# Kernel optimization log

Hardware: AMD Instinct MI355X
Metric: run time of the kernel (lower is better)

Reference implementation:

```python
import jax, jax.numpy as jnp
import numpy as np

T, IN, H, OUT = 4096, 1024, 2048, 1024


def setup_inputs() -> dict:
    key = jax.random.key(0)
    ks = jax.random.split(key, 7)
    s_x = np.float32(np.sqrt(2.0 / (IN + H)))   # Wx init scale
    s_h = np.float32(np.sqrt(1.0 / H))          # Wh init scale
    s_y = np.float32(np.sqrt(2.0 / (H + OUT)))  # Wy init scale
    return {
        "x": jax.random.normal(ks[0], (T, IN), jnp.float32),
        "Wx_f": jax.random.normal(ks[1], (H, IN), jnp.float32) * s_x,
        "Wh_f": jax.random.normal(ks[2], (H, H), jnp.float32) * s_h,
        "bh_f": jnp.zeros((H,), jnp.float32),
        "Wx_b": jax.random.normal(ks[3], (H, IN), jnp.float32) * s_x,
        "Wh_b": jax.random.normal(ks[4], (H, H), jnp.float32) * s_h,
        "bh_b": jnp.zeros((H,), jnp.float32),
        "Wy_f": jax.random.normal(ks[5], (OUT, H), jnp.float32) * s_y,
        "Wy_b": jax.random.normal(ks[6], (OUT, H), jnp.float32) * s_y,
        "by": jnp.zeros((OUT,), jnp.float32),
    }


def reference(x, Wx_f, Wh_f, bh_f, Wx_b, Wh_b, bh_b, Wy_f, Wy_b, by):
    # Precompute input projections for all timesteps (batched GEMM): [T, H]
    xWf = x @ Wx_f.T + bh_f
    xWb = x @ Wx_b.T + bh_b
    h0 = jnp.zeros((Wh_f.shape[0],), x.dtype)

    def make_step(Wh):
        def step(h, xw):
            h = jnp.tanh(xw + h @ Wh.T)
            return h, h
        return step

    # Forward direction: h_t = tanh(Wx x_t + Wh h_{t-1} + bh)
    _, hf = jax.lax.scan(make_step(Wh_f), h0, xWf)
    # Backward direction: same recurrence scanned from t=T-1 down to 0;
    # reverse=True yields outputs stacked in original time order,
    # matching h_backward_hist[::-1] in the torch code.
    _, hb = jax.lax.scan(make_step(Wh_b), h0, xWb, reverse=True)

    # Output per timestep: Wy_f h_f + Wy_b h_b + by -> [T, OUT], flattened
    y = hf @ Wy_f.T + hb @ Wy_b.T + by
    return y.reshape(-1)
```

## Files before the change

kernel.cpp:

```cpp
#include <hip/hip_runtime.h>
#include <hip/hip_bf16.h>
#include <math.h>

#define T_N   4096
#define IN_N  1024
#define H_N   2048
#define OUT_N 1024

#define KD3  64
#define RPB3 32
#define RTH3 1024

#define XW_F_OFF 0ull
#define XW_B_OFF 33554432ull
#define HF_OFF   67108864ull
#define HB_OFF   100663296ull
#define PROG_OFF 134217728ull

__global__ __launch_bounds__(128) void init_prog_kernel(unsigned* __restrict__ p) {
  p[threadIdx.x] = 0u;
}

__global__ __launch_bounds__(256) void gemm_xw_kernel(
    const float* __restrict__ x,
    const float* __restrict__ Wxf, const float* __restrict__ bhf,
    const float* __restrict__ Wxb, const float* __restrict__ bhb,
    float* __restrict__ xwf, float* __restrict__ xwb)
{
  const int dir = blockIdx.z;
  const float* __restrict__ B    = dir ? Wxb : Wxf;
  const float* __restrict__ bias = dir ? bhb : bhf;
  float* __restrict__ C          = dir ? xwb : xwf;
  const int bm0 = blockIdx.y * 64;
  const int bn0 = blockIdx.x * 64;

  __shared__ float As[16][65];
  __shared__ float Bs[16][65];
  const int tid  = threadIdx.x;
  const int ty   = tid >> 4, tx = tid & 15;
  const int lrow = tid >> 2, lkq = (tid & 3) << 2;
  float acc[4][4] = {};

  for (int k0 = 0; k0 < IN_N; k0 += 16) {
    float4 a4 = *(const float4*)(x + (size_t)(bm0 + lrow) * IN_N + k0 + lkq);
    float4 b4 = *(const float4*)(B + (size_t)(bn0 + lrow) * IN_N + k0 + lkq);
    As[lkq + 0][lrow] = a4.x; As[lkq + 1][lrow] = a4.y;
    As[lkq + 2][lrow] = a4.z; As[lkq + 3][lrow] = a4.w;
    Bs[lkq + 0][lrow] = b4.x; Bs[lkq + 1][lrow] = b4.y;
    Bs[lkq + 2][lrow] = b4.z; Bs[lkq + 3][lrow] = b4.w;
    __syncthreads();
#pragma unroll
    for (int k = 0; k < 16; ++k) {
      float a[4], b[4];
#pragma unroll
      for (int i = 0; i < 4; ++i) a[i] = As[k][ty * 4 + i];
#pragma unroll
      for (int j = 0; j < 4; ++j) b[j] = Bs[k][tx * 4 + j];
#pragma unroll
      for (int i = 0; i < 4; ++i)
#pragma unroll
        for (int j = 0; j < 4; ++j) acc[i][j] = fmaf(a[i], b[j], acc[i][j]);
    }
    __syncthreads();
  }
#pragma unroll
  for (int i = 0; i < 4; ++i) {
    float4 v;
    v.x = acc[i][0] + bias[bn0 + tx * 4 + 0];
    v.y = acc[i][1] + bias[bn0 + tx * 4 + 1];
    v.z = acc[i][2] + bias[bn0 + tx * 4 + 2];
    v.w = acc[i][3] + bias[bn0 + tx * 4 + 3];
    *(float4*)(C + (size_t)(bm0 + ty * 4 + i) * H_N + bn0 + tx * 4) = v;
  }
}

__global__ __launch_bounds__(256) void gemm_out_kernel(
    const float* __restrict__ hf, const float* __restrict__ hb,
    const float* __restrict__ Wyf, const float* __restrict__ Wyb,
    const float* __restrict__ by, float* __restrict__ y)
{
  const int bm0 = blockIdx.y * 64;
  const int bn0 = blockIdx.x * 64;
  __shared__ float As[16][65];
  __shared__ float Bs[16][65];
  const int tid  = threadIdx.x;
  const int ty   = tid >> 4, tx = tid & 15;
  const int lrow = tid >> 2, lkq = (tid & 3) << 2;
  float acc[4][4] = {};

#pragma unroll 1
  for (int pass = 0; pass < 2; ++pass) {
    const float* __restrict__ A = pass ? hb : hf;
    const float* __restrict__ B = pass ? Wyb : Wyf;
    for (int k0 = 0; k0 < H_N; k0 += 16) {
      float4 a4 = *(const float4*)(A + (size_t)(bm0 + lrow) * H_N + k0 + lkq);
      float4 b4 = *(const float4*)(B + (size_t)(bn0 + lrow) * H_N + k0 + lkq);
      As[lkq + 0][lrow] = a4.x; As[lkq + 1][lrow] = a4.y;
      As[lkq + 2][lrow] = a4.z; As[lkq + 3][lrow] = a4.w;
      Bs[lkq + 0][lrow] = b4.x; Bs[lkq + 1][lrow] = b4.y;
      Bs[lkq + 2][lrow] = b4.z; Bs[lkq + 3][lrow] = b4.w;
      __syncthreads();
#pragma unroll
      for (int k = 0; k < 16; ++k) {
        float a[4], b[4];
#pragma unroll
        for (int i = 0; i < 4; ++i) a[i] = As[k][ty * 4 + i];
#pragma unroll
        for (int j = 0; j < 4; ++j) b[j] = Bs[k][tx * 4 + j];
#pragma unroll
        for (int i = 0; i < 4; ++i)
#pragma unroll
          for (int j = 0; j < 4; ++j) acc[i][j] = fmaf(a[i], b[j], acc[i][j]);
      }
      __syncthreads();
    }
  }
#pragma unroll
  for (int i = 0; i < 4; ++i) {
    float4 v;
    v.x = acc[i][0] + by[bn0 + tx * 4 + 0];
    v.y = acc[i][1] + by[bn0 + tx * 4 + 1];
    v.z = acc[i][2] + by[bn0 + tx * 4 + 2];
    v.w = acc[i][3] + by[bn0 + tx * 4 + 3];
    *(float4*)(y + (size_t)(bm0 + ty * 4 + i) * OUT_N + bn0 + tx * 4) = v;
  }
}

__global__ __launch_bounds__(RTH3, 4) void recurrent_kernel(
    const float* __restrict__ Whf, const float* __restrict__ Whb,
    const float* __restrict__ xwf, const float* __restrict__ xwb,
    float* __restrict__ hf, float* __restrict__ hb,
    unsigned* __restrict__ progf, unsigned* __restrict__ progb)
{
  const int b    = blockIdx.x;
  const bool fwd = (b < KD3);
  const int bb   = fwd ? b : b - KD3;
  const int rb   = bb * RPB3;
  const float* __restrict__ Wh = fwd ? Whf : Whb;
  const float* __restrict__ xw = fwd ? xwf : xwb;
  float* __restrict__ hist     = fwd ? hf : hb;
  unsigned* __restrict__ prog  = fwd ? progf : progb;

  const int w     = threadIdx.x >> 6;
  const int lane  = threadIdx.x & 63;
  const int jbase = lane << 2;
  const int r0    = rb + 2 * w;

  __shared__ __align__(16) float hs[H_N];

  float4 wv[2][8];
#pragma unroll
  for (int q = 0; q < 2; ++q)
#pragma unroll
    for (int k = 0; k < 8; ++k)
      wv[q][k] = *(const float4*)(Wh + (size_t)(r0 + q) * H_N + k * 256 + jbase);
#pragma unroll
  for (int q = 0; q < 2; ++q)
#pragma unroll
    for (int k = 0; k < 8; ++k)
      asm volatile("" : "+v"(wv[q][k].x), "+v"(wv[q][k].y),
                        "+v"(wv[q][k].z), "+v"(wv[q][k].w));

  for (int s = 0; s < T_N; ++s) {
    const int t  = fwd ? s : (T_N - 1 - s);
    const int pt = fwd ? (t - 1) : (t + 1);

    float xwv0 = 0.f, xwv1 = 0.f;
    if (lane == 0) {
      xwv0 = xw[(size_t)t * H_N + r0 + 0];
      xwv1 = xw[(size_t)t * H_N + r0 + 1];
    }

    if (s > 0) {
      if (w == 0) {
        for (;;) {
          unsigned p = __hip_atomic_load(prog + lane, __ATOMIC_RELAXED,
                                         __HIP_MEMORY_SCOPE_AGENT);
          if (__all(p >= (unsigned)s)) break;
          __builtin_amdgcn_s_sleep(1);
        }
        asm volatile("" ::: "memory");
      }
      __syncthreads();
      unsigned long long hv2 = __hip_atomic_load(
          (const unsigned long long*)(hist + (size_t)pt * H_N) + threadIdx.x,
          __ATOMIC_RELAXED, __HIP_MEMORY_SCOPE_AGENT);
      *((unsigned long long*)hs + threadIdx.x) = hv2;
      __syncthreads();
    } else {
      *((unsigned long long*)hs + threadIdx.x) = 0ull;
      __syncthreads();
    }

    float acc0 = 0.f, acc1 = 0.f;
#pragma unroll
    for (int k = 0; k < 8; ++k) {
      float4 h4 = *(const float4*)(hs + k * 256 + jbase);
      acc0 = fmaf(wv[0][k].x, h4.x, acc0);
      acc0 = fmaf(wv[0][k].y, h4.y, acc0);
      acc0 = fmaf(wv[0][k].z, h4.z, acc0);
      acc0 = fmaf(wv[0][k].w, h4.w, acc0);
      acc1 = fmaf(wv[1][k].x, h4.x, acc1);
      acc1 = fmaf(wv[1][k].y, h4.y, acc1);
      acc1 = fmaf(wv[1][k].z, h4.z, acc1);
      acc1 = fmaf(wv[1][k].w, h4.w, acc1);
    }
#pragma unroll
    for (int off = 32; off > 0; off >>= 1) {
      acc0 += __shfl_xor(acc0, off, 64);
      acc1 += __shfl_xor(acc1, off, 64);
    }

    if (lane == 0) {
      union { float f; unsigned u; } h0, h1;
      h0.f = tanhf(acc0 + xwv0);
      h1.f = tanhf(acc1 + xwv1);
      unsigned* hu = (unsigned*)(hist + (size_t)t * H_N + r0);
      __hip_atomic_store(hu + 0, h0.u, __ATOMIC_RELAXED, __HIP_MEMORY_SCOPE_AGENT);
      __hip_atomic_store(hu + 1, h1.u, __ATOMIC_RELAXED, __HIP_MEMORY_SCOPE_AGENT);
    }

    __syncthreads();
    if (threadIdx.x == 0)
      __hip_atomic_store(prog + bb, (unsigned)(s + 1), __ATOMIC_RELAXED,
                         __HIP_MEMORY_SCOPE_AGENT);
  }
}

extern "C" void kernel_launch(void* const* d_in, const int* in_sizes, int n_in,
                              void* d_out, int out_size, void* d_ws, size_t ws_size,
                              hipStream_t stream) {
  const float* x   = (const float*)d_in[0];
  const float* Wxf = (const float*)d_in[1];
  const float* Whf = (const float*)d_in[2];
  const float* bhf = (const float*)d_in[3];
  const float* Wxb = (const float*)d_in[4];
  const float* Whb = (const float*)d_in[5];
  const float* bhb = (const float*)d_in[6];
  const float* Wyf = (const float*)d_in[7];
  const float* Wyb = (const float*)d_in[8];
  const float* by  = (const float*)d_in[9];
  float* y = (float*)d_out;

  char* ws = (char*)d_ws;
  float* xwf      = (float*)(ws + XW_F_OFF);
  float* xwb      = (float*)(ws + XW_B_OFF);
  float* hf       = (float*)(ws + HF_OFF);
  float* hb       = (float*)(ws + HB_OFF);
  unsigned* progf = (unsigned*)(ws + PROG_OFF);
  unsigned* progb = progf + 64;

  hipLaunchKernelGGL(init_prog_kernel, dim3(1), dim3(128), 0, stream, progf);
  hipLaunchKernelGGL(gemm_xw_kernel, dim3(H_N / 64, T_N / 64, 2), dim3(256), 0, stream,
                     x, Wxf, bhf, Wxb, bhb, xwf, xwb);
  hipLaunchKernelGGL(recurrent_kernel, dim3(2 * KD3), dim3(RTH3), 0, stream,
                     Whf, Whb, xwf, xwb, hf, hb, progf, progb);
  hipLaunchKernelGGL(gemm_out_kernel, dim3(OUT_N / 64, T_N / 64), dim3(256), 0, stream,
                     hf, hb, Wyf, Wyb, by, y);
}
```

Measured before the change: 12.46 ms.

## Replace progress-counter barrier with sentinel-filled history polling

Drops the per-block progress counters and has each thread poll its own slice of the previous hidden-state vector until the 0xFFFFFFFF sentinel is overwritten. The history buffers are pre-filled with the sentinel by a new fill kernel. This removes one barrier, the counter store after each step, and the serialized wave-0 spin followed by a separate load, so cross-block synchronization goes straight through the data. In exchange the kernel must write 64MB of sentinel values up front, and it relies on tanh outputs never matching the sentinel bit pattern (a NaN) and on relaxed-ordering visibility of the data itself.

```diff
diff --git a/kernel.cpp b/kernel.cpp
--- a/kernel.cpp
+++ b/kernel.cpp
@@ -11,14 +11,19 @@
 #define RPB3 32
 #define RTH3 1024
 
+#define SENT 0xFFFFFFFFu
+
 #define XW_F_OFF 0ull
 #define XW_B_OFF 33554432ull
 #define HF_OFF   67108864ull
 #define HB_OFF   100663296ull
-#define PROG_OFF 134217728ull
-
-__global__ __launch_bounds__(128) void init_prog_kernel(unsigned* __restrict__ p) {
-  p[threadIdx.x] = 0u;
+
+__global__ __launch_bounds__(256) void sentinel_fill_kernel(ulonglong2* __restrict__ p) {
+  const unsigned long long n = (64ull << 20) / 16ull;
+  ulonglong2 v; v.x = 0xFFFFFFFFFFFFFFFFull; v.y = 0xFFFFFFFFFFFFFFFFull;
+  for (unsigned long long i = blockIdx.x * 256ull + threadIdx.x; i < n;
+       i += gridDim.x * 256ull)
+    p[i] = v;
 }
 
 __global__ __launch_bounds__(256) void gemm_xw_kernel(
@@ -129,8 +134,7 @@
 __global__ __launch_bounds__(RTH3, 4) void recurrent_kernel(
     const float* __restrict__ Whf, const float* __restrict__ Whb,
     const float* __restrict__ xwf, const float* __restrict__ xwb,
-    float* __restrict__ hf, float* __restrict__ hb,
-    unsigned* __restrict__ progf, unsigned* __restrict__ progb)
+    float* __restrict__ hf, float* __restrict__ hb)
 {
   const int b    = blockIdx.x;
   const bool fwd = (b < KD3);
@@ -139,7 +143,6 @@
   const float* __restrict__ Wh = fwd ? Whf : Whb;
   const float* __restrict__ xw = fwd ? xwf : xwb;
   float* __restrict__ hist     = fwd ? hf : hb;
-  unsigned* __restrict__ prog  = fwd ? progf : progb;
 
   const int w     = threadIdx.x >> 6;
   const int lane  = threadIdx.x & 63;
@@ -172,25 +175,19 @@
     }
 
     if (s > 0) {
-      if (w == 0) {
-        for (;;) {
-          unsigned p = __hip_atomic_load(prog + lane, __ATOMIC_RELAXED,
-                                         __HIP_MEMORY_SCOPE_AGENT);
-          if (__all(p >= (unsigned)s)) break;
-          __builtin_amdgcn_s_sleep(1);
-        }
-        asm volatile("" ::: "memory");
+      const unsigned long long* src =
+          (const unsigned long long*)(hist + (size_t)pt * H_N) + threadIdx.x;
+      unsigned long long hv2;
+      for (;;) {
+        hv2 = __hip_atomic_load(src, __ATOMIC_RELAXED, __HIP_MEMORY_SCOPE_AGENT);
+        if ((unsigned)hv2 != SENT && (unsigned)(hv2 >> 32) != SENT) break;
+        __builtin_amdgcn_s_sleep(1);
       }
-      __syncthreads();
-      unsigned long long hv2 = __hip_atomic_load(
-          (const unsigned long long*)(hist + (size_t)pt * H_N) + threadIdx.x,
-          __ATOMIC_RELAXED, __HIP_MEMORY_SCOPE_AGENT);
       *((unsigned long long*)hs + threadIdx.x) = hv2;
-      __syncthreads();
     } else {
       *((unsigned long long*)hs + threadIdx.x) = 0ull;
-      __syncthreads();
-    }
+    }
+    __syncthreads();
 
     float acc0 = 0.f, acc1 = 0.f;
 #pragma unroll
@@ -221,9 +218,6 @@
     }
 
     __syncthreads();
-    if (threadIdx.x == 0)
-      __hip_atomic_store(prog + bb, (unsigned)(s + 1), __ATOMIC_RELAXED,
-                         __HIP_MEMORY_SCOPE_AGENT);
   }
 }
 
@@ -243,18 +237,17 @@
   float* y = (float*)d_out;
 
   char* ws = (char*)d_ws;
-  float* xwf      = (float*)(ws + XW_F_OFF);
-  float* xwb      = (float*)(ws + XW_B_OFF);
-  float* hf       = (float*)(ws + HF_OFF);
-  float* hb       = (float*)(ws + HB_OFF);
-  unsigned* progf = (unsigned*)(ws + PROG_OFF);
-  unsigned* progb = progf + 64;
-
-  hipLaunchKernelGGL(init_prog_kernel, dim3(1), dim3(128), 0, stream, progf);
+  float* xwf = (float*)(ws + XW_F_OFF);
+  float* xwb = (float*)(ws + XW_B_OFF);
+  float* hf  = (float*)(ws + HF_OFF);
+  float* hb  = (float*)(ws + HB_OFF);
+
+  hipLaunchKernelGGL(sentinel_fill_kernel, dim3(1024), dim3(256), 0, stream,
+                     (ulonglong2*)(ws + HF_OFF));
   hipLaunchKernelGGL(gemm_xw_kernel, dim3(H_N / 64, T_N / 64, 2), dim3(256), 0, stream,
                      x, Wxf, bhf, Wxb, bhb, xwf, xwb);
   hipLaunchKernelGGL(recurrent_kernel, dim3(2 * KD3), dim3(RTH3), 0, stream,
-                     Whf, Whb, xwf, xwb, hf, hb, progf, progb);
+                     Whf, Whb, xwf, xwb, hf, hb);
   hipLaunchKernelGGL(gemm_out_kernel, dim3(OUT_N / 64, T_N / 64), dim3(256), 0, stream,
                      hf, hb, Wyf, Wyb, by, y);
 }
```

Measured after the change: 15.76 ms. +26.6%, slower.

## Halve recurrent block threads and give each wave four rows

Applied to the files above, without the earlier changes.

The recurrent kernel now runs 512 threads per block, with each wave computing four output rows instead of two. The wave keeps twice as many Wh registers, and the hidden-state load into shared memory is split into two 64-bit atomics per thread. The xw values are read with one float4 and the new h values are written as two 64-bit atomic stores. The sleep in the spin-wait is removed. Together these aim to cut per-step barrier and wave-coordination cost in a latency-bound recurrence, at the price of higher register pressure and more memory traffic from polling.

```diff
diff --git a/kernel.cpp b/kernel.cpp
--- a/kernel.cpp
+++ b/kernel.cpp
@@ -9,7 +9,7 @@
 
 #define KD3  64
 #define RPB3 32
-#define RTH3 1024
+#define RTH3 512
 
 #define XW_F_OFF 0ull
 #define XW_B_OFF 33554432ull
@@ -126,7 +126,7 @@
   }
 }
 
-__global__ __launch_bounds__(RTH3, 4) void recurrent_kernel(
+__global__ __launch_bounds__(RTH3, 2) void recurrent_kernel(
     const float* __restrict__ Whf, const float* __restrict__ Whb,
     const float* __restrict__ xwf, const float* __restrict__ xwb,
     float* __restrict__ hf, float* __restrict__ hb,
@@ -144,18 +144,18 @@
   const int w     = threadIdx.x >> 6;
   const int lane  = threadIdx.x & 63;
   const int jbase = lane << 2;
-  const int r0    = rb + 2 * w;
+  const int r0    = rb + 4 * w;
 
   __shared__ __align__(16) float hs[H_N];
 
-  float4 wv[2][8];
-#pragma unroll
-  for (int q = 0; q < 2; ++q)
+  float4 wv[4][8];
+#pragma unroll
+  for (int q = 0; q < 4; ++q)
 #pragma unroll
     for (int k = 0; k < 8; ++k)
       wv[q][k] = *(const float4*)(Wh + (size_t)(r0 + q) * H_N + k * 256 + jbase);
 #pragma unroll
-  for (int q = 0; q < 2; ++q)
+  for (int q = 0; q < 4; ++q)
 #pragma unroll
     for (int k = 0; k < 8; ++k)
       asm volatile("" : "+v"(wv[q][k].x), "+v"(wv[q][k].y),
@@ -165,11 +165,9 @@
     const int t  = fwd ? s : (T_N - 1 - s);
     const int pt = fwd ? (t - 1) : (t + 1);
 
-    float xwv0 = 0.f, xwv1 = 0.f;
-    if (lane == 0) {
-      xwv0 = xw[(size_t)t * H_N + r0 + 0];
-      xwv1 = xw[(size_t)t * H_N + r0 + 1];
-    }
+    float4 xwv = make_float4(0.f, 0.f, 0.f, 0.f);
+    if (lane == 0)
+      xwv = *(const float4*)(xw + (size_t)t * H_N + r0);
 
     if (s > 0) {
       if (w == 0) {
@@ -177,47 +175,57 @@
           unsigned p = __hip_atomic_load(prog + lane, __ATOMIC_RELAXED,
                                          __HIP_MEMORY_SCOPE_AGENT);
           if (__all(p >= (unsigned)s)) break;
-          __builtin_amdgcn_s_sleep(1);
         }
         asm volatile("" ::: "memory");
       }
       __syncthreads();
-      unsigned long long hv2 = __hip_atomic_load(
-          (const unsigned long long*)(hist + (size_t)pt * H_N) + threadIdx.x,
+      const unsigned long long* src =
+          (const unsigned long long*)(hist + (size_t)pt * H_N);
+      unsigned long long h0 = __hip_atomic_load(src + 2 * threadIdx.x + 0,
           __ATOMIC_RELAXED, __HIP_MEMORY_SCOPE_AGENT);
-      *((unsigned long long*)hs + threadIdx.x) = hv2;
-      __syncthreads();
+      unsigned long long h1 = __hip_atomic_load(src + 2 * threadIdx.x + 1,
+          __ATOMIC_RELAXED, __HIP_MEMORY_SCOPE_AGENT);
+      ((unsigned long long*)hs)[2 * threadIdx.x + 0] = h0;
+      ((unsigned long long*)hs)[2 * threadIdx.x + 1] = h1;
     } else {
-      *((unsigned long long*)hs + threadIdx.x) = 0ull;
-      __syncthreads();
-    }
-
-    float acc0 = 0.f, acc1 = 0.f;
+      ((unsigned long long*)hs)[2 * threadIdx.x + 0] = 0ull;
+      ((unsigned long long*)hs)[2 * threadIdx.x + 1] = 0ull;
+    }
+    __syncthreads();
+
+    float acc0 = 0.f, acc1 = 0.f, acc2 = 0.f, acc3 = 0.f;
 #pragma unroll
     for (int k = 0; k < 8; ++k) {
       float4 h4 = *(const float4*)(hs + k * 256 + jbase);
-      acc0 = fmaf(wv[0][k].x, h4.x, acc0);
-      acc0 = fmaf(wv[0][k].y, h4.y, acc0);
-      acc0 = fmaf(wv[0][k].z, h4.z, acc0);
-      acc0 = fmaf(wv[0][k].w, h4.w, acc0);
-      acc1 = fmaf(wv[1][k].x, h4.x, acc1);
-      acc1 = fmaf(wv[1][k].y, h4.y, acc1);
-      acc1 = fmaf(wv[1][k].z, h4.z, acc1);
-      acc1 = fmaf(wv[1][k].w, h4.w, acc1);
+      acc0 = fmaf(wv[0][k].x, h4.x, acc0); acc0 = fmaf(wv[0][k].y, h4.y, acc0);
+      acc0 = fmaf(wv[0][k].z, h4.z, acc0); acc0 = fmaf(wv[0][k].w, h4.w, acc0);
+      acc1 = fmaf(wv[1][k].x, h4.x, acc1); acc1 = fmaf(wv[1][k].y, h4.y, acc1);
+      acc1 = fmaf(wv[1][k].z, h4.z, acc1); acc1 = fmaf(wv[1][k].w, h4.w, acc1);
+      acc2 = fmaf(wv[2][k].x, h4.x, acc2); acc2 = fmaf(wv[2][k].y, h4.y, acc2);
+      acc2 = fmaf(wv[2][k].z, h4.z, acc2); acc2 = fmaf(wv[2][k].w, h4.w, acc2);
+      acc3 = fmaf(wv[3][k].x, h4.x, acc3); acc3 = fmaf(wv[3][k].y, h4.y, acc3);
+      acc3 = fmaf(wv[3][k].z, h4.z, acc3); acc3 = fmaf(wv[3][k].w, h4.w, acc3);
     }
 #pragma unroll
     for (int off = 32; off > 0; off >>= 1) {
       acc0 += __shfl_xor(acc0, off, 64);
       acc1 += __shfl_xor(acc1, off, 64);
+      acc2 += __shfl_xor(acc2, off, 64);
+      acc3 += __shfl_xor(acc3, off, 64);
     }
 
     if (lane == 0) {
-      union { float f; unsigned u; } h0, h1;
-      h0.f = tanhf(acc0 + xwv0);
-      h1.f = tanhf(acc1 + xwv1);
-      unsigned* hu = (unsigned*)(hist + (size_t)t * H_N + r0);
-      __hip_atomic_store(hu + 0, h0.u, __ATOMIC_RELAXED, __HIP_MEMORY_SCOPE_AGENT);
-      __hip_atomic_store(hu + 1, h1.u, __ATOMIC_RELAXED, __HIP_MEMORY_SCOPE_AGENT);
+      union { float f; unsigned u; } r[4];
+      r[0].f = tanhf(acc0 + xwv.x);
+      r[1].f = tanhf(acc1 + xwv.y);
+      r[2].f = tanhf(acc2 + xwv.z);
+      r[3].f = tanhf(acc3 + xwv.w);
+      unsigned long long p0 = ((unsigned long long)r[1].u << 32) | r[0].u;
+      unsigned long long p1 = ((unsigned long long)r[3].u << 32) | r[2].u;
+      unsigned long long* dst =
+          (unsigned long long*)(hist + (size_t)t * H_N + r0);
+      __hip_atomic_store(dst + 0, p0, __ATOMIC_RELAXED, __HIP_MEMORY_SCOPE_AGENT);
+      __hip_atomic_store(dst + 1, p1, __ATOMIC_RELAXED, __HIP_MEMORY_SCOPE_AGENT);
     }
 
     __syncthreads();
```

After: 13.14 ms. 1.05x slower.

## Fuse input-projection GEMM into recurrent kernel with per-chunk readiness counters

Applied to the files above, without the earlier changes.

Merges the input-projection GEMM and the recurrent scan into one persistent kernel. 128 blocks run the recurrence while 1024 extra blocks compute xW tiles. Each 64-timestep chunk bumps a counter when its tiles are done, so the recurrence can start on early chunks instead of waiting for the whole GEMM. The backward direction computes chunks in reverse order to match its scan. This hides GEMM time behind the latency-bound recurrence. The risks are GEMM blocks competing with recurrent blocks for compute units, and deadlock if the recurrent blocks are not all co-resident.

```diff
diff --git a/kernel.cpp b/kernel.cpp
--- a/kernel.cpp
+++ b/kernel.cpp
@@ -7,9 +7,11 @@
 #define H_N   2048
 #define OUT_N 1024
 
-#define KD3  64
-#define RPB3 32
-#define RTH3 1024
+#define KD   64
+#define RPB  32
+#define RTH  1024
+#define NREC 128
+#define NGEMM 1024
 
 #define XW_F_OFF 0ull
 #define XW_B_OFF 33554432ull
@@ -17,60 +19,183 @@
 #define HB_OFF   100663296ull
 #define PROG_OFF 134217728ull
 
-__global__ __launch_bounds__(128) void init_prog_kernel(unsigned* __restrict__ p) {
+__global__ __launch_bounds__(256) void init_prog_kernel(unsigned* __restrict__ p) {
   p[threadIdx.x] = 0u;
 }
 
-__global__ __launch_bounds__(256) void gemm_xw_kernel(
+__global__ __launch_bounds__(RTH, 4) void mega_kernel(
     const float* __restrict__ x,
     const float* __restrict__ Wxf, const float* __restrict__ bhf,
     const float* __restrict__ Wxb, const float* __restrict__ bhb,
-    float* __restrict__ xwf, float* __restrict__ xwb)
+    const float* __restrict__ Whf, const float* __restrict__ Whb,
+    float* __restrict__ xwf, float* __restrict__ xwb,
+    float* __restrict__ hf, float* __restrict__ hb,
+    unsigned* __restrict__ prog)
 {
-  const int dir = blockIdx.z;
-  const float* __restrict__ B    = dir ? Wxb : Wxf;
-  const float* __restrict__ bias = dir ? bhb : bhf;
-  float* __restrict__ C          = dir ? xwb : xwf;
-  const int bm0 = blockIdx.y * 64;
-  const int bn0 = blockIdx.x * 64;
-
-  __shared__ float As[16][65];
-  __shared__ float Bs[16][65];
-  const int tid  = threadIdx.x;
-  const int ty   = tid >> 4, tx = tid & 15;
-  const int lrow = tid >> 2, lkq = (tid & 3) << 2;
-  float acc[4][4] = {};
-
-  for (int k0 = 0; k0 < IN_N; k0 += 16) {
-    float4 a4 = *(const float4*)(x + (size_t)(bm0 + lrow) * IN_N + k0 + lkq);
-    float4 b4 = *(const float4*)(B + (size_t)(bn0 + lrow) * IN_N + k0 + lkq);
-    As[lkq + 0][lrow] = a4.x; As[lkq + 1][lrow] = a4.y;
-    As[lkq + 2][lrow] = a4.z; As[lkq + 3][lrow] = a4.w;
-    Bs[lkq + 0][lrow] = b4.x; Bs[lkq + 1][lrow] = b4.y;
-    Bs[lkq + 2][lrow] = b4.z; Bs[lkq + 3][lrow] = b4.w;
+  __shared__ __align__(16) float hs[H_N];
+  __shared__ float As[4][16][65];
+  __shared__ float Bs[4][16][65];
+
+  const int b = blockIdx.x;
+  if (b < NREC) {
+    const bool fwd = (b < KD);
+    const int bb   = fwd ? b : b - KD;
+    const int rb   = bb * RPB;
+    const float* __restrict__ Wh = fwd ? Whf : Whb;
+    const float* __restrict__ xw = fwd ? xwf : xwb;
+    float* __restrict__ hist     = fwd ? hf : hb;
+    unsigned* __restrict__ flg   = prog + (fwd ? 0 : 64);
+    unsigned* __restrict__ cnt   = prog + (fwd ? 128 : 192);
+
+    const int w     = threadIdx.x >> 6;
+    const int lane  = threadIdx.x & 63;
+    const int jbase = lane << 2;
+    const int r0    = rb + 2 * w;
+
+    float4 wv[2][8];
+#pragma unroll
+    for (int q = 0; q < 2; ++q)
+#pragma unroll
+      for (int k = 0; k < 8; ++k)
+        wv[q][k] = *(const float4*)(Wh + (size_t)(r0 + q) * H_N + k * 256 + jbase);
+#pragma unroll
+    for (int q = 0; q < 2; ++q)
+#pragma unroll
+      for (int k = 0; k < 8; ++k)
+        asm volatile("" : "+v"(wv[q][k].x), "+v"(wv[q][k].y),
+                          "+v"(wv[q][k].z), "+v"(wv[q][k].w));
+
+    for (int s = 0; s < T_N; ++s) {
+      const int t  = fwd ? s : (T_N - 1 - s);
+      const int pt = fwd ? (t - 1) : (t + 1);
+      const int chunk = t >> 6;
+
+      if (w == 0) {
+        for (;;) {
+          unsigned p = (s > 0)
+              ? __hip_atomic_load(flg + lane, __ATOMIC_RELAXED,
+                                  __HIP_MEMORY_SCOPE_AGENT)
+              : (unsigned)s;
+          unsigned c = __hip_atomic_load(cnt + chunk, __ATOMIC_RELAXED,
+                                         __HIP_MEMORY_SCOPE_AGENT);
+          if (__all(p >= (unsigned)s && c >= 32u)) break;
+          __builtin_amdgcn_s_sleep(1);
+        }
+        asm volatile("" ::: "memory");
+      }
+      __syncthreads();
+
+      if (s > 0) {
+        unsigned long long hv2 = __hip_atomic_load(
+            (const unsigned long long*)(hist + (size_t)pt * H_N) + threadIdx.x,
+            __ATOMIC_RELAXED, __HIP_MEMORY_SCOPE_AGENT);
+        *((unsigned long long*)hs + threadIdx.x) = hv2;
+      } else {
+        *((unsigned long long*)hs + threadIdx.x) = 0ull;
+      }
+      float xwv0 = 0.f, xwv1 = 0.f;
+      if (lane == 0) {
+        unsigned long long xq = __hip_atomic_load(
+            (const unsigned long long*)(xw + (size_t)t * H_N + r0),
+            __ATOMIC_RELAXED, __HIP_MEMORY_SCOPE_AGENT);
+        xwv0 = __uint_as_float((unsigned)xq);
+        xwv1 = __uint_as_float((unsigned)(xq >> 32));
+      }
+      __syncthreads();
+
+      float acc0 = 0.f, acc1 = 0.f;
+#pragma unroll
+      for (int k = 0; k < 8; ++k) {
+        float4 h4 = *(const float4*)(hs + k * 256 + jbase);
+        acc0 = fmaf(wv[0][k].x, h4.x, acc0);
+        acc0 = fmaf(wv[0][k].y, h4.y, acc0);
+        acc0 = fmaf(wv[0][k].z, h4.z, acc0);
+        acc0 = fmaf(wv[0][k].w, h4.w, acc0);
+        acc1 = fmaf(wv[1][k].x, h4.x, acc1);
+        acc1 = fmaf(wv[1][k].y, h4.y, acc1);
+        acc1 = fmaf(wv[1][k].z, h4.z, acc1);
+        acc1 = fmaf(wv[1][k].w, h4.w, acc1);
+      }
+#pragma unroll
+      for (int off = 32; off > 0; off >>= 1) {
+        acc0 += __shfl_xor(acc0, off, 64);
+        acc1 += __shfl_xor(acc1, off, 64);
+      }
+
+      if (lane == 0) {
+        union { float f; unsigned u; } h0, h1;
+        h0.f = tanhf(acc0 + xwv0);
+        h1.f = tanhf(acc1 + xwv1);
+        unsigned* hu = (unsigned*)(hist + (size_t)t * H_N + r0);
+        __hip_atomic_store(hu + 0, h0.u, __ATOMIC_RELAXED, __HIP_MEMORY_SCOPE_AGENT);
+        __hip_atomic_store(hu + 1, h1.u, __ATOMIC_RELAXED, __HIP_MEMORY_SCOPE_AGENT);
+      }
+
+      __syncthreads();
+      if (threadIdx.x == 0)
+        __hip_atomic_store(flg + bb, (unsigned)(s + 1), __ATOMIC_RELAXED,
+                           __HIP_MEMORY_SCOPE_AGENT);
+    }
+  } else {
+    const int gid  = b - NREC;
+    const int dir  = gid & 1;
+    const int rr   = gid >> 1;
+    int bm = rr >> 3;
+    if (dir) bm = 63 - bm;
+    const int quad = rr & 7;
+    const int grp  = threadIdx.x >> 8;
+    const int tid  = threadIdx.x & 255;
+    const float* __restrict__ B    = dir ? Wxb : Wxf;
+    const float* __restrict__ bias = dir ? bhb : bhf;
+    float* __restrict__ C          = dir ? xwb : xwf;
+    unsigned* __restrict__ cnt     = prog + (dir ? 192 : 128);
+    const int bm0 = bm * 64;
+    const int bn0 = (quad * 4 + grp) * 64;
+
+    const int ty = tid >> 4, tx = tid & 15;
+    const int lrow = tid >> 2, lkq = (tid & 3) << 2;
+    float acc[4][4] = {};
+
+    for (int k0 = 0; k0 < IN_N; k0 += 16) {
+      float4 a4 = *(const float4*)(x + (size_t)(bm0 + lrow) * IN_N + k0 + lkq);
+      float4 b4 = *(const float4*)(B + (size_t)(bn0 + lrow) * IN_N + k0 + lkq);
+      As[grp][lkq + 0][lrow] = a4.x; As[grp][lkq + 1][lrow] = a4.y;
+      As[grp][lkq + 2][lrow] = a4.z; As[grp][lkq + 3][lrow] = a4.w;
+      Bs[grp][lkq + 0][lrow] = b4.x; Bs[grp][lkq + 1][lrow] = b4.y;
+      Bs[grp][lkq + 2][lrow] = b4.z; Bs[grp][lkq + 3][lrow] = b4.w;
+      __syncthreads();
+#pragma unroll
+      for (int k = 0; k < 16; ++k) {
+        float a[4], bv[4];
+#pragma unroll
+        for (int i = 0; i < 4; ++i) a[i] = As[grp][k][ty * 4 + i];
+#pragma unroll
+        for (int j = 0; j < 4; ++j) bv[j] = Bs[grp][k][tx * 4 + j];
+#pragma unroll
+        for (int i = 0; i < 4; ++i)
+#pragma unroll
+          for (int j = 0; j < 4; ++j) acc[i][j] = fmaf(a[i], bv[j], acc[i][j]);
+      }
+      __syncthreads();
+    }
+#pragma unroll
+    for (int i = 0; i < 4; ++i) {
+      union { float f; unsigned u; } v[4];
+      v[0].f = acc[i][0] + bias[bn0 + tx * 4 + 0];
+      v[1].f = acc[i][1] + bias[bn0 + tx * 4 + 1];
+      v[2].f = acc[i][2] + bias[bn0 + tx * 4 + 2];
+      v[3].f = acc[i][3] + bias[bn0 + tx * 4 + 3];
+      unsigned long long p0 = ((unsigned long long)v[1].u << 32) | v[0].u;
+      unsigned long long p1 = ((unsigned long long)v[3].u << 32) | v[2].u;
+      unsigned long long* dst = (unsigned long long*)
+          (C + (size_t)(bm0 + ty * 4 + i) * H_N + bn0 + tx * 4);
+      __hip_atomic_store(dst + 0, p0, __ATOMIC_RELAXED, __HIP_MEMORY_SCOPE_AGENT);
+      __hip_atomic_store(dst + 1, p1, __ATOMIC_RELAXED, __HIP_MEMORY_SCOPE_AGENT);
+    }
     __syncthreads();
-#pragma unroll
-    for (int k = 0; k < 16; ++k) {
-      float a[4], b[4];
-#pragma unroll
-      for (int i = 0; i < 4; ++i) a[i] = As[k][ty * 4 + i];
-#pragma unroll
-      for (int j = 0; j < 4; ++j) b[j] = Bs[k][tx * 4 + j];
-#pragma unroll
-      for (int i = 0; i < 4; ++i)
-#pragma unroll
-        for (int j = 0; j < 4; ++j) acc[i][j] = fmaf(a[i], b[j], acc[i][j]);
-    }
-    __syncthreads();
-  }
-#pragma unroll
-  for (int i = 0; i < 4; ++i) {
-    float4 v;
-    v.x = acc[i][0] + bias[bn0 + tx * 4 + 0];
-    v.y = acc[i][1] + bias[bn0 + tx * 4 + 1];
-    v.z = acc[i][2] + bias[bn0 + tx * 4 + 2];
-    v.w = acc[i][3] + bias[bn0 + tx * 4 + 3];
-    *(float4*)(C + (size_t)(bm0 + ty * 4 + i) * H_N + bn0 + tx * 4) = v;
+    if (threadIdx.x == 0)
+      __hip_atomic_fetch_add(cnt + bm, 4u, __ATOMIC_RELAXED,
+                             __HIP_MEMORY_SCOPE_AGENT);
   }
 }
 
@@ -102,15 +227,15 @@
       __syncthreads();
 #pragma unroll
       for (int k = 0; k < 16; ++k) {
-        float a[4], b[4];
+        float a[4], bv[4];
 #pragma unroll
         for (int i = 0; i < 4; ++i) a[i] = As[k][ty * 4 + i];
 #pragma unroll
-        for (int j = 0; j < 4; ++j) b[j] = Bs[k][tx * 4 + j];
+        for (int j = 0; j < 4; ++j) bv[j] = Bs[k][tx * 4 + j];
 #pragma unroll
         for (int i = 0; i < 4; ++i)
 #pragma unroll
-          for (int j = 0; j < 4; ++j) acc[i][j] = fmaf(a[i], b[j], acc[i][j]);
+          for (int j = 0; j < 4; ++j) acc[i][j] = fmaf(a[i], bv[j], acc[i][j]);
       }
       __syncthreads();
     }
@@ -123,107 +248,6 @@
     v.z = acc[i][2] + by[bn0 + tx * 4 + 2];
     v.w = acc[i][3] + by[bn0 + tx * 4 + 3];
     *(float4*)(y + (size_t)(bm0 + ty * 4 + i) * OUT_N + bn0 + tx * 4) = v;
-  }
-}
-
-__global__ __launch_bounds__(RTH3, 4) void recurrent_kernel(
-    const float* __restrict__ Whf, const float* __restrict__ Whb,
-    const float* __restrict__ xwf, const float* __restrict__ xwb,
-    float* __restrict__ hf, float* __restrict__ hb,
-    unsigned* __restrict__ progf, unsigned* __restrict__ progb)
-{
-  const int b    = blockIdx.x;
-  const bool fwd = (b < KD3);
-  const int bb   = fwd ? b : b - KD3;
-  const int rb   = bb * RPB3;
-  const float* __restrict__ Wh = fwd ? Whf : Whb;
-  const float* __restrict__ xw = fwd ? xwf : xwb;
-  float* __restrict__ hist     = fwd ? hf : hb;
-  unsigned* __restrict__ prog  = fwd ? progf : progb;
-
-  const int w     = threadIdx.x >> 6;
-  const int lane  = threadIdx.x & 63;
-  const int jbase = lane << 2;
-  const int r0    = rb + 2 * w;
-
-  __shared__ __align__(16) float hs[H_N];
-
-  float4 wv[2][8];
-#pragma unroll
-  for (int q = 0; q < 2; ++q)
-#pragma unroll
-    for (int k = 0; k < 8; ++k)
-      wv[q][k] = *(const float4*)(Wh + (size_t)(r0 + q) * H_N + k * 256 + jbase);
-#pragma unroll
-  for (int q = 0; q < 2; ++q)
-#pragma unroll
-    for (int k = 0; k < 8; ++k)
-      asm volatile("" : "+v"(wv[q][k].x), "+v"(wv[q][k].y),
-                        "+v"(wv[q][k].z), "+v"(wv[q][k].w));
-
-  for (int s = 0; s < T_N; ++s) {
-    const int t  = fwd ? s : (T_N - 1 - s);
-    const int pt = fwd ? (t - 1) : (t + 1);
-
-    float xwv0 = 0.f, xwv1 = 0.f;
-    if (lane == 0) {
-      xwv0 = xw[(size_t)t * H_N + r0 + 0];
-      xwv1 = xw[(size_t)t * H_N + r0 + 1];
-    }
-
-    if (s > 0) {
-      if (w == 0) {
-        for (;;) {
-          unsigned p = __hip_atomic_load(prog + lane, __ATOMIC_RELAXED,
-                                         __HIP_MEMORY_SCOPE_AGENT);
-          if (__all(p >= (unsigned)s)) break;
-          __builtin_amdgcn_s_sleep(1);
-        }
-        asm volatile("" ::: "memory");
-      }
-      __syncthreads();
-      unsigned long long hv2 = __hip_atomic_load(
-          (const unsigned long long*)(hist + (size_t)pt * H_N) + threadIdx.x,
-          __ATOMIC_RELAXED, __HIP_MEMORY_SCOPE_AGENT);
-      *((unsigned long long*)hs + threadIdx.x) = hv2;
-      __syncthreads();
-    } else {
-      *((unsigned long long*)hs + threadIdx.x) = 0ull;
-      __syncthreads();
-    }
-
-    float acc0 = 0.f, acc1 = 0.f;
-#pragma unroll
-    for (int k = 0; k < 8; ++k) {
-      float4 h4 = *(const float4*)(hs + k * 256 + jbase);
-      acc0 = fmaf(wv[0][k].x, h4.x, acc0);
-      acc0 = fmaf(wv[0][k].y, h4.y, acc0);
-      acc0 = fmaf(wv[0][k].z, h4.z, acc0);
-      acc0 = fmaf(wv[0][k].w, h4.w, acc0);
-      acc1 = fmaf(wv[1][k].x, h4.x, acc1);
-      acc1 = fmaf(wv[1][k].y, h4.y, acc1);
-      acc1 = fmaf(wv[1][k].z, h4.z, acc1);
-      acc1 = fmaf(wv[1][k].w, h4.w, acc1);
-    }
-#pragma unroll
-    for (int off = 32; off > 0; off >>= 1) {
-      acc0 += __shfl_xor(acc0, off, 64);
-      acc1 += __shfl_xor(acc1, off, 64);
-    }
-
-    if (lane == 0) {
-      union { float f; unsigned u; } h0, h1;
-      h0.f = tanhf(acc0 + xwv0);
-      h1.f = tanhf(acc1 + xwv1);
-      unsigned* hu = (unsigned*)(hist + (size_t)t * H_N + r0);
-      __hip_atomic_store(hu + 0, h0.u, __ATOMIC_RELAXED, __HIP_MEMORY_SCOPE_AGENT);
-      __hip_atomic_store(hu + 1, h1.u, __ATOMIC_RELAXED, __HIP_MEMORY_SCOPE_AGENT);
-    }
-
-    __syncthreads();
-    if (threadIdx.x == 0)
-      __hip_atomic_store(prog + bb, (unsigned)(s + 1), __ATOMIC_RELAXED,
-                         __HIP_MEMORY_SCOPE_AGENT);
   }
 }
 
@@ -243,18 +267,15 @@
   float* y = (float*)d_out;
 
   char* ws = (char*)d_ws;
-  float* xwf      = (float*)(ws + XW_F_OFF);
-  float* xwb      = (float*)(ws + XW_B_OFF);
-  float* hf       = (float*)(ws + HF_OFF);
-  float* hb       = (float*)(ws + HB_OFF);
-  unsigned* progf = (unsigned*)(ws + PROG_OFF);
-  unsigned* progb = progf + 64;
-
-  hipLaunchKernelGGL(init_prog_kernel, dim3(1), dim3(128), 0, stream, progf);
-  hipLaunchKernelGGL(gemm_xw_kernel, dim3(H_N / 64, T_N / 64, 2), dim3(256), 0, stream,
-                     x, Wxf, bhf, Wxb, bhb, xwf, xwb);
-  hipLaunchKernelGGL(recurrent_kernel, dim3(2 * KD3), dim3(RTH3), 0, stream,
-                     Whf, Whb, xwf, xwb, hf, hb, progf, progb);
+  float* xwf     = (float*)(ws + XW_F_OFF);
+  float* xwb     = (float*)(ws + XW_B_OFF);
+  float* hf      = (float*)(ws + HF_OFF);
+  float* hb      = (float*)(ws + HB_OFF);
+  unsigned* prog = (unsigned*)(ws + PROG_OFF);
+
+  hipLaunchKernelGGL(init_prog_kernel, dim3(1), dim3(256), 0, stream, prog);
+  hipLaunchKernelGGL(mega_kernel, dim3(NREC + NGEMM), dim3(RTH), 0, stream,
+                     x, Wxf, bhf, Wxb, bhb, Whf, Whb, xwf, xwb, hf, hb, prog);
   hipLaunchKernelGGL(gemm_out_kernel, dim3(OUT_N / 64, T_N / 64), dim3(256), 0, stream,
                      hf, hb, Wyf, Wyb, by, y);
 }
```

Result: slower. 18.49 ms (+48.5%).
